# Optimization experiments

Hardware: AMD Instinct MI355X
Metric: run time of the kernel (lower is better)

## Reference

```python
import jax, jax.numpy as jnp
import numpy as np

N = 50000
E = 1600000
NEG_SLOPE = 0.2


def gat_layer(x, src, dst, e_attr, w_fc, w_e, ah, ae, at, b, H, F, act):
    # node projection: [N, H, F]
    feat = (x @ w_fc.T).reshape(N, H, F)
    eh = (feat * ah).sum(-1)          # [N, H] attn_h . feat_src
    et = (feat * at).sum(-1)          # [N, H] attn_t . feat_dst (same feats, homogeneous graph)
    # edge projection: [E, H, F]
    fe = (e_attr @ w_e.T).reshape(E, H, F)
    ee = (fe * ae).sum(-1)            # [E, H]
    # per-edge score: u_add_e then e_add_v, leaky relu
    e = eh[src] + ee + et[dst]        # [E, H]
    e = jnp.where(e > 0, e, NEG_SLOPE * e)
    # edge softmax over incoming edges of each dst node
    m = jax.ops.segment_max(e, dst, num_segments=N)      # [N, H]
    ex = jnp.exp(e - m[dst])
    s = jax.ops.segment_sum(ex, dst, num_segments=N)     # [N, H]
    a = ex / s[dst]                   # [E, H]
    # weighted aggregation: u_mul_e -> sum over incoming edges
    msg = feat[src] * a[:, :, None]   # [E, H, F]
    out = jax.ops.segment_sum(msg, dst, num_segments=N)  # [N, H, F]
    out = out + b.reshape(1, H, F)
    out = out.reshape(N, H * F)       # concat_out=True
    if act:
        out = jax.nn.relu(out)
    return out


def setup_inputs() -> dict:
    key = jax.random.key(0)
    ks = jax.random.split(key, 16)
    d = {}
    d['x'] = jax.random.normal(ks[0], (N, 128), dtype=jnp.float32)
    d['edge_attr'] = jax.random.normal(ks[1], (E, 64), dtype=jnp.float32)
    d['src'] = jax.random.randint(ks[2], (E,), 0, N, dtype=jnp.int32)
    d['dst'] = jax.random.randint(ks[3], (E,), 0, N, dtype=jnp.int32)
    # layer 1: in=128, H=4, F=32
    d['w_fc1'] = jax.random.normal(ks[4], (128, 128), dtype=jnp.float32) * 0.1
    d['w_e1'] = jax.random.normal(ks[5], (128, 64), dtype=jnp.float32) * 0.1
    d['ah1'] = jax.random.normal(ks[6], (4, 32), dtype=jnp.float32) * 0.1
    d['ae1'] = jax.random.normal(ks[7], (4, 32), dtype=jnp.float32) * 0.1
    d['at1'] = jax.random.normal(ks[8], (4, 32), dtype=jnp.float32) * 0.1
    d['b1'] = jnp.zeros((128,), dtype=jnp.float32)
    # layer 2: in=128, H=1, F=64
    d['w_fc2'] = jax.random.normal(ks[9], (64, 128), dtype=jnp.float32) * 0.1
    d['w_e2'] = jax.random.normal(ks[10], (64, 64), dtype=jnp.float32) * 0.1
    d['ah2'] = jax.random.normal(ks[11], (1, 64), dtype=jnp.float32) * 0.1
    d['ae2'] = jax.random.normal(ks[12], (1, 64), dtype=jnp.float32) * 0.1
    d['at2'] = jax.random.normal(ks[13], (1, 64), dtype=jnp.float32) * 0.1
    d['b2'] = jnp.zeros((64,), dtype=jnp.float32)
    return d


def reference(x, edge_attr, src, dst,
              w_fc1, w_e1, ah1, ae1, at1, b1,
              w_fc2, w_e2, ah2, ae2, at2, b2):
    h = gat_layer(x, src, dst, edge_attr, w_fc1, w_e1, ah1, ae1, at1, b1, 4, 32, True)
    h = gat_layer(h, src, dst, edge_attr, w_fc2, w_e2, ah2, ae2, at2, b2, 1, 64, False)
    return h
```

## Files before the change

kernel.cpp:

```cpp
#include <hip/hip_runtime.h>

#define NEG_SLOPE 0.2f

__global__ void hist_k(const int* __restrict__ dst, int* __restrict__ counts,
                       int* __restrict__ pos, int E) {
    int i = blockIdx.x * blockDim.x + threadIdx.x;
    if (i < E) pos[i] = atomicAdd(&counts[dst[i]], 1);
}

__global__ __launch_bounds__(256) void scan_blocks(const int* __restrict__ in,
                                                   int* __restrict__ part,
                                                   int* __restrict__ aux, int n) {
    __shared__ int wsum[4];
    int t = threadIdx.x;
    int lane = t & 63;
    int w = t >> 6;
    int base = blockIdx.x * 1024 + t * 4;
    int c[4];
#pragma unroll
    for (int i = 0; i < 4; ++i) c[i] = (base + i < n) ? in[base + i] : 0;
    int tsum = c[0] + c[1] + c[2] + c[3];
    int incl = tsum;
#pragma unroll
    for (int d = 1; d < 64; d <<= 1) {
        int v = __shfl_up(incl, d, 64);
        if (lane >= d) incl += v;
    }
    if (lane == 63) wsum[w] = incl;
    __syncthreads();
    int wpre = 0;
    for (int i = 0; i < w; ++i) wpre += wsum[i];
    int run = wpre + incl - tsum;
#pragma unroll
    for (int i = 0; i < 4; ++i) {
        if (base + i < n) part[base + i] = run;
        run += c[i];
    }
    if (t == 255) aux[blockIdx.x] = run;
}

__global__ void scan_aux_k(int* __restrict__ aux, int* __restrict__ offs, int nblk, int N) {
    int t = threadIdx.x;
    int v = (t < nblk) ? aux[t] : 0;
    int incl = v;
#pragma unroll
    for (int d = 1; d < 64; d <<= 1) {
        int u = __shfl_up(incl, d, 64);
        if (t >= d) incl += u;
    }
    if (t < nblk) aux[t] = incl - v;
    if (t == 63) offs[N] = incl;
}

__global__ void scan_add_k(int* __restrict__ offs, const int* __restrict__ aux, int n) {
    int i = blockIdx.x * blockDim.x + threadIdx.x;
    if (i < n) offs[i] += aux[i >> 10];
}

__global__ void prep_we(const float* __restrict__ ae1, const float* __restrict__ we1,
                        const float* __restrict__ ae2, const float* __restrict__ we2,
                        float* __restrict__ wec) {
    int t = threadIdx.x;
    if (t < 256) {
        int h = t >> 6, c = t & 63;
        float s = 0.f;
        for (int f = 0; f < 32; ++f) s = fmaf(ae1[h * 32 + f], we1[(h * 32 + f) * 64 + c], s);
        wec[h * 64 + c] = s;
    } else if (t < 320) {
        int c = t - 256;
        float s = 0.f;
        for (int f = 0; f < 64; ++f) s = fmaf(ae2[f], we2[f * 64 + c], s);
        wec[256 + c] = s;
    }
}

__global__ __launch_bounds__(256) void edge_proj_csr(const float* __restrict__ ea,
                                                     const float* __restrict__ wec,
                                                     const float* __restrict__ eh1,
                                                     const int* __restrict__ src,
                                                     const int* __restrict__ dst,
                                                     const int* __restrict__ pos,
                                                     const int* __restrict__ offs,
                                                     float* __restrict__ pe1,
                                                     float* __restrict__ ee2c,
                                                     int* __restrict__ esrc, int E) {
    __shared__ float w[5][64];
    for (int i = threadIdx.x; i < 320; i += 256) w[i / 64][i % 64] = wec[i];
    __syncthreads();
    int e = blockIdx.x * blockDim.x + threadIdx.x;
    if (e >= E) return;
    const float4* row = (const float4*)(ea + (size_t)e * 64);
    float acc[5] = {0.f, 0.f, 0.f, 0.f, 0.f};
#pragma unroll
    for (int q = 0; q < 16; ++q) {
        float4 v = row[q];
#pragma unroll
        for (int h = 0; h < 5; ++h) {
            float4 wv = *(const float4*)&w[h][4 * q];
            acc[h] = fmaf(v.x, wv.x, acc[h]);
            acc[h] = fmaf(v.y, wv.y, acc[h]);
            acc[h] = fmaf(v.z, wv.z, acc[h]);
            acc[h] = fmaf(v.w, wv.w, acc[h]);
        }
    }
    int s = src[e];
    int p = offs[dst[e]] + pos[e];
    float4 ehv = *(const float4*)(eh1 + (size_t)s * 4);
    *(float4*)(pe1 + (size_t)p * 4) =
        make_float4(acc[0] + ehv.x, acc[1] + ehv.y, acc[2] + ehv.z, acc[3] + ehv.w);
    ee2c[p] = acc[4];
    esrc[p] = s;
}

template <int M>
__global__ __launch_bounds__(256) void gemm_nodes(const float* __restrict__ X,
                                                  const float* __restrict__ W,
                                                  float* __restrict__ out, int N) {
    const int K = 128, KC = 64, NT = 64;
    __shared__ float xs[NT][KC + 1];
    __shared__ float ws[KC][M + 1];
    const int CT = M / 8;
    const int NG = 256 / CT;
    const int NPT = NT / NG;
    int t = threadIdx.x;
    int tc = t % CT, tn = t / CT;
    int nb = blockIdx.x * NT;
    float acc[NPT][8];
#pragma unroll
    for (int i = 0; i < NPT; ++i)
#pragma unroll
        for (int j = 0; j < 8; ++j) acc[i][j] = 0.f;

    for (int kc = 0; kc < K; kc += KC) {
        for (int i = t * 4; i < M * KC; i += 1024) {
            int m = i / KC, k = i % KC;
            float4 v = *(const float4*)(W + (size_t)m * K + kc + k);
            ws[k][m] = v.x; ws[k + 1][m] = v.y; ws[k + 2][m] = v.z; ws[k + 3][m] = v.w;
        }
        for (int i = t * 4; i < NT * KC; i += 1024) {
            int r = i / KC, k = i % KC;
            int n = nb + r;
            float4 v = make_float4(0.f, 0.f, 0.f, 0.f);
            if (n < N) v = *(const float4*)(X + (size_t)n * K + kc + k);
            xs[r][k] = v.x; xs[r][k + 1] = v.y; xs[r][k + 2] = v.z; xs[r][k + 3] = v.w;
        }
        __syncthreads();
#pragma unroll 4
        for (int k = 0; k < KC; ++k) {
            float wv[8];
            *(float4*)&wv[0] = *(const float4*)&ws[k][tc * 8];
            *(float4*)&wv[4] = *(const float4*)&ws[k][tc * 8 + 4];
#pragma unroll
            for (int i = 0; i < NPT; ++i) {
                float xv = xs[tn * NPT + i][k];
#pragma unroll
                for (int j = 0; j < 8; ++j) acc[i][j] = fmaf(xv, wv[j], acc[i][j]);
            }
        }
        __syncthreads();
    }
#pragma unroll
    for (int i = 0; i < NPT; ++i) {
        int n = nb + tn * NPT + i;
        if (n < N) {
            *(float4*)(out + (size_t)n * M + tc * 8) =
                make_float4(acc[i][0], acc[i][1], acc[i][2], acc[i][3]);
            *(float4*)(out + (size_t)n * M + tc * 8 + 4) =
                make_float4(acc[i][4], acc[i][5], acc[i][6], acc[i][7]);
        }
    }
}

template <int H, int F>
__global__ void ehet(const float* __restrict__ feat, const float* __restrict__ ah,
                     const float* __restrict__ at, float* __restrict__ eh,
                     float* __restrict__ et, int N) {
    int i = blockIdx.x * blockDim.x + threadIdx.x;
    if (i >= N * H) return;
    int h = i % H;
    const float* f = feat + (size_t)i * F;
    float sh = 0.f, st = 0.f;
#pragma unroll
    for (int j = 0; j < F; j += 4) {
        float4 v = *(const float4*)(f + j);
        float4 a = *(const float4*)(ah + h * F + j);
        float4 b = *(const float4*)(at + h * F + j);
        sh += v.x * a.x + v.y * a.y + v.z * a.z + v.w * a.w;
        st += v.x * b.x + v.y * b.y + v.z * b.z + v.w * b.w;
    }
    eh[i] = sh;
    et[i] = st;
}

__global__ __launch_bounds__(256) void agg1(const float* __restrict__ feat,
                                            const float* __restrict__ pe1,
                                            const float* __restrict__ et,
                                            const int* __restrict__ offs,
                                            const int* __restrict__ esrc,
                                            const float* __restrict__ bias,
                                            float* __restrict__ out, int N) {
    int n = (blockIdx.x * blockDim.x + threadIdx.x) >> 6;
    int l = threadIdx.x & 63;
    if (n >= N) return;
    int start = offs[n], end = offs[n + 1];
    int eg = l >> 3, li = l & 7, h = li >> 1;
    float etv = et[n * 4 + h];

    float s = 0.f;
    float4 a0 = make_float4(0.f, 0.f, 0.f, 0.f);
    float4 a1 = a0, a2 = a0, a3 = a0;
    for (int j0 = start; j0 < end; j0 += 8) {
        int j = j0 + eg;
        if (j < end) {
            int sv = esrc[j];
            float x = pe1[(size_t)j * 4 + h] + etv;
            x = x > 0.f ? x : NEG_SLOPE * x;
            float wgt = __expf(x);
            s += wgt;
            const float4* fr = (const float4*)(feat + (size_t)sv * 128 + li * 16);
            float4 v0 = fr[0], v1 = fr[1], v2 = fr[2], v3 = fr[3];
            a0.x = fmaf(wgt, v0.x, a0.x); a0.y = fmaf(wgt, v0.y, a0.y);
            a0.z = fmaf(wgt, v0.z, a0.z); a0.w = fmaf(wgt, v0.w, a0.w);
            a1.x = fmaf(wgt, v1.x, a1.x); a1.y = fmaf(wgt, v1.y, a1.y);
            a1.z = fmaf(wgt, v1.z, a1.z); a1.w = fmaf(wgt, v1.w, a1.w);
            a2.x = fmaf(wgt, v2.x, a2.x); a2.y = fmaf(wgt, v2.y, a2.y);
            a2.z = fmaf(wgt, v2.z, a2.z); a2.w = fmaf(wgt, v2.w, a2.w);
            a3.x = fmaf(wgt, v3.x, a3.x); a3.y = fmaf(wgt, v3.y, a3.y);
            a3.z = fmaf(wgt, v3.z, a3.z); a3.w = fmaf(wgt, v3.w, a3.w);
        }
    }
#pragma unroll
    for (int d = 8; d < 64; d <<= 1) {
        s += __shfl_xor(s, d);
        a0.x += __shfl_xor(a0.x, d); a0.y += __shfl_xor(a0.y, d);
        a0.z += __shfl_xor(a0.z, d); a0.w += __shfl_xor(a0.w, d);
        a1.x += __shfl_xor(a1.x, d); a1.y += __shfl_xor(a1.y, d);
        a1.z += __shfl_xor(a1.z, d); a1.w += __shfl_xor(a1.w, d);
        a2.x += __shfl_xor(a2.x, d); a2.y += __shfl_xor(a2.y, d);
        a2.z += __shfl_xor(a2.z, d); a2.w += __shfl_xor(a2.w, d);
        a3.x += __shfl_xor(a3.x, d); a3.y += __shfl_xor(a3.y, d);
        a3.z += __shfl_xor(a3.z, d); a3.w += __shfl_xor(a3.w, d);
    }
    if (eg == 0) {
        float inv = s > 0.f ? 1.f / s : 0.f;
        const float4* bp = (const float4*)(bias + li * 16);
        float4 b0 = bp[0], b1 = bp[1], b2 = bp[2], b3 = bp[3];
        float4* op = (float4*)(out + (size_t)n * 128 + li * 16);
        op[0] = make_float4(fmaxf(a0.x * inv + b0.x, 0.f), fmaxf(a0.y * inv + b0.y, 0.f),
                            fmaxf(a0.z * inv + b0.z, 0.f), fmaxf(a0.w * inv + b0.w, 0.f));
        op[1] = make_float4(fmaxf(a1.x * inv + b1.x, 0.f), fmaxf(a1.y * inv + b1.y, 0.f),
                            fmaxf(a1.z * inv + b1.z, 0.f), fmaxf(a1.w * inv + b1.w, 0.f));
        op[2] = make_float4(fmaxf(a2.x * inv + b2.x, 0.f), fmaxf(a2.y * inv + b2.y, 0.f),
                            fmaxf(a2.z * inv + b2.z, 0.f), fmaxf(a2.w * inv + b2.w, 0.f));
        op[3] = make_float4(fmaxf(a3.x * inv + b3.x, 0.f), fmaxf(a3.y * inv + b3.y, 0.f),
                            fmaxf(a3.z * inv + b3.z, 0.f), fmaxf(a3.w * inv + b3.w, 0.f));
    }
}

__global__ __launch_bounds__(256) void agg2(const float* __restrict__ feat,
                                            const float* __restrict__ ee2c,
                                            const float* __restrict__ eh2,
                                            const float* __restrict__ et2,
                                            const int* __restrict__ offs,
                                            const int* __restrict__ esrc,
                                            const float* __restrict__ bias,
                                            float* __restrict__ out, int N) {
    int n = (blockIdx.x * blockDim.x + threadIdx.x) >> 6;
    int l = threadIdx.x & 63;
    if (n >= N) return;
    int start = offs[n], end = offs[n + 1];
    int eg = l >> 3, li = l & 7;
    float etv = et2[n];

    float s = 0.f;
    float4 a0 = make_float4(0.f, 0.f, 0.f, 0.f);
    float4 a1 = a0;
    for (int j0 = start; j0 < end; j0 += 8) {
        int j = j0 + eg;
        if (j < end) {
            int sv = esrc[j];
            float x = eh2[sv] + ee2c[j] + etv;
            x = x > 0.f ? x : NEG_SLOPE * x;
            float wgt = __expf(x);
            s += wgt;
            const float4* fr = (const float4*)(feat + (size_t)sv * 64 + li * 8);
            float4 v0 = fr[0], v1 = fr[1];
            a0.x = fmaf(wgt, v0.x, a0.x); a0.y = fmaf(wgt, v0.y, a0.y);
            a0.z = fmaf(wgt, v0.z, a0.z); a0.w = fmaf(wgt, v0.w, a0.w);
            a1.x = fmaf(wgt, v1.x, a1.x); a1.y = fmaf(wgt, v1.y, a1.y);
            a1.z = fmaf(wgt, v1.z, a1.z); a1.w = fmaf(wgt, v1.w, a1.w);
        }
    }
#pragma unroll
    for (int d = 8; d < 64; d <<= 1) {
        s += __shfl_xor(s, d);
        a0.x += __shfl_xor(a0.x, d); a0.y += __shfl_xor(a0.y, d);
        a0.z += __shfl_xor(a0.z, d); a0.w += __shfl_xor(a0.w, d);
        a1.x += __shfl_xor(a1.x, d); a1.y += __shfl_xor(a1.y, d);
        a1.z += __shfl_xor(a1.z, d); a1.w += __shfl_xor(a1.w, d);
    }
    if (eg == 0) {
        float inv = s > 0.f ? 1.f / s : 0.f;
        const float4* bp = (const float4*)(bias + li * 8);
        float4 b0 = bp[0], b1 = bp[1];
        float4* op = (float4*)(out + (size_t)n * 64 + li * 8);
        op[0] = make_float4(a0.x * inv + b0.x, a0.y * inv + b0.y,
                            a0.z * inv + b0.z, a0.w * inv + b0.w);
        op[1] = make_float4(a1.x * inv + b1.x, a1.y * inv + b1.y,
                            a1.z * inv + b1.z, a1.w * inv + b1.w);
    }
}

extern "C" void kernel_launch(void* const* d_in, const int* in_sizes, int n_in,
                              void* d_out, int out_size, void* d_ws, size_t ws_size,
                              hipStream_t stream) {
    const float* x    = (const float*)d_in[0];
    const float* ea   = (const float*)d_in[1];
    const int*   src  = (const int*)d_in[2];
    const int*   dst  = (const int*)d_in[3];
    const float* wfc1 = (const float*)d_in[4];
    const float* we1  = (const float*)d_in[5];
    const float* ah1  = (const float*)d_in[6];
    const float* ae1  = (const float*)d_in[7];
    const float* at1  = (const float*)d_in[8];
    const float* b1   = (const float*)d_in[9];
    const float* wfc2 = (const float*)d_in[10];
    const float* we2  = (const float*)d_in[11];
    const float* ah2  = (const float*)d_in[12];
    const float* ae2  = (const float*)d_in[13];
    const float* at2  = (const float*)d_in[14];
    const float* b2   = (const float*)d_in[15];
    const int N = in_sizes[0] / 128;
    const int E = in_sizes[2];
    float* out = (float*)d_out;

    char* p = (char*)d_ws;
    auto alloc = [&](size_t bytes) -> void* {
        void* r = (void*)p;
        p += (bytes + 255) & ~(size_t)255;
        return r;
    };
    int*   counts = (int*)alloc((size_t)N * 4);
    int*   offs   = (int*)alloc(((size_t)N + 1) * 4);
    int*   aux    = (int*)alloc(64 * 4);
    int*   pos    = (int*)alloc((size_t)E * 4);
    float* wec    = (float*)alloc(320 * 4);
    float* pe1    = (float*)alloc((size_t)E * 4 * 4);
    float* ee2c   = (float*)alloc((size_t)E * 4);
    int*   esrc   = (int*)alloc((size_t)E * 4);
    float* feat1  = (float*)alloc((size_t)N * 128 * 4);
    float* eh1    = (float*)alloc((size_t)N * 4 * 4);
    float* et1    = (float*)alloc((size_t)N * 4 * 4);
    float* h1     = (float*)alloc((size_t)N * 128 * 4);
    float* feat2  = (float*)alloc((size_t)N * 64 * 4);
    float* eh2    = (float*)alloc((size_t)N * 4);
    float* et2    = (float*)alloc((size_t)N * 4);

    int ebl = (E + 255) / 256;
    int nblk = (N + 1023) / 1024;

    hipMemsetAsync(counts, 0, (size_t)N * 4, stream);
    hist_k<<<ebl, 256, 0, stream>>>(dst, counts, pos, E);
    scan_blocks<<<nblk, 256, 0, stream>>>(counts, offs, aux, N);
    scan_aux_k<<<1, 64, 0, stream>>>(aux, offs, nblk, N);
    scan_add_k<<<(N + 255) / 256, 256, 0, stream>>>(offs, aux, N);

    gemm_nodes<128><<<(N + 63) / 64, 256, 0, stream>>>(x, wfc1, feat1, N);
    ehet<4, 32><<<(N * 4 + 255) / 256, 256, 0, stream>>>(feat1, ah1, at1, eh1, et1, N);

    prep_we<<<1, 320, 0, stream>>>(ae1, we1, ae2, we2, wec);
    edge_proj_csr<<<ebl, 256, 0, stream>>>(ea, wec, eh1, src, dst, pos, offs,
                                           pe1, ee2c, esrc, E);

    agg1<<<(N + 3) / 4, 256, 0, stream>>>(feat1, pe1, et1, offs, esrc, b1, h1, N);

    gemm_nodes<64><<<(N + 63) / 64, 256, 0, stream>>>(h1, wfc2, feat2, N);
    ehet<1, 64><<<(N + 255) / 256, 256, 0, stream>>>(feat2, ah2, at2, eh2, et2, N);
    agg2<<<(N + 3) / 4, 256, 0, stream>>>(feat2, ee2c, eh2, et2, offs, esrc, b2, out, N);
}
```

Baseline: 1.064 ms.

## Coalesce edge projection: 16 lanes per edge row with shuffle reduction

Rewrites the edge projection so each group of 16 lanes reads one 64-float edge row as contiguous float4 loads, with weights held in registers, and reduces the five dot products with xor shuffles. It uses a grid-stride loop over a fixed 4096-block grid, with four edges per lane group per iteration to keep several loads in flight. This targets the uncoalesced per-thread row reads of the 410MB edge_attr stream. The cost is extra shuffle work and lane-0-only scatter stores. A shuffle order swap in agg1 is cosmetic.

Measured after the change: 1.025 ms. -3.7%, faster.

```diff
diff --git a/kernel.cpp b/kernel.cpp
--- a/kernel.cpp
+++ b/kernel.cpp
@@ -84,32 +84,54 @@
                                                      float* __restrict__ pe1,
                                                      float* __restrict__ ee2c,
                                                      int* __restrict__ esrc, int E) {
-    __shared__ float w[5][64];
-    for (int i = threadIdx.x; i < 320; i += 256) w[i / 64][i % 64] = wec[i];
-    __syncthreads();
-    int e = blockIdx.x * blockDim.x + threadIdx.x;
-    if (e >= E) return;
-    const float4* row = (const float4*)(ea + (size_t)e * 64);
-    float acc[5] = {0.f, 0.f, 0.f, 0.f, 0.f};
-#pragma unroll
-    for (int q = 0; q < 16; ++q) {
-        float4 v = row[q];
-#pragma unroll
-        for (int h = 0; h < 5; ++h) {
-            float4 wv = *(const float4*)&w[h][4 * q];
-            acc[h] = fmaf(v.x, wv.x, acc[h]);
-            acc[h] = fmaf(v.y, wv.y, acc[h]);
-            acc[h] = fmaf(v.z, wv.z, acc[h]);
-            acc[h] = fmaf(v.w, wv.w, acc[h]);
-        }
-    }
-    int s = src[e];
-    int p = offs[dst[e]] + pos[e];
-    float4 ehv = *(const float4*)(eh1 + (size_t)s * 4);
-    *(float4*)(pe1 + (size_t)p * 4) =
-        make_float4(acc[0] + ehv.x, acc[1] + ehv.y, acc[2] + ehv.z, acc[3] + ehv.w);
-    ee2c[p] = acc[4];
-    esrc[p] = s;
+    int l = threadIdx.x & 63;
+    int li = l & 15;
+    int eg = l >> 4;
+    int wid = (blockIdx.x * blockDim.x + threadIdx.x) >> 6;
+    int nw = (gridDim.x * blockDim.x) >> 6;
+    float4 w0 = *(const float4*)(wec + 0 * 64 + li * 4);
+    float4 w1 = *(const float4*)(wec + 1 * 64 + li * 4);
+    float4 w2 = *(const float4*)(wec + 2 * 64 + li * 4);
+    float4 w3 = *(const float4*)(wec + 3 * 64 + li * 4);
+    float4 w4 = *(const float4*)(wec + 4 * 64 + li * 4);
+    int nq = (E + 3) >> 2;
+    for (int q0 = wid * 4; q0 < nq; q0 += nw * 4) {
+        float4 v[4];
+        int e[4];
+#pragma unroll
+        for (int u = 0; u < 4; ++u) {
+            e[u] = (q0 + u) * 4 + eg;
+            v[u] = make_float4(0.f, 0.f, 0.f, 0.f);
+            if (e[u] < E) v[u] = *(const float4*)(ea + (size_t)e[u] * 64 + li * 4);
+        }
+#pragma unroll
+        for (int u = 0; u < 4; ++u) {
+            float4 vv = v[u];
+            float d0 = fmaf(vv.x, w0.x, fmaf(vv.y, w0.y, fmaf(vv.z, w0.z, vv.w * w0.w)));
+            float d1 = fmaf(vv.x, w1.x, fmaf(vv.y, w1.y, fmaf(vv.z, w1.z, vv.w * w1.w)));
+            float d2 = fmaf(vv.x, w2.x, fmaf(vv.y, w2.y, fmaf(vv.z, w2.z, vv.w * w2.w)));
+            float d3 = fmaf(vv.x, w3.x, fmaf(vv.y, w3.y, fmaf(vv.z, w3.z, vv.w * w3.w)));
+            float d4 = fmaf(vv.x, w4.x, fmaf(vv.y, w4.y, fmaf(vv.z, w4.z, vv.w * w4.w)));
+#pragma unroll
+            for (int m = 1; m < 16; m <<= 1) {
+                d0 += __shfl_xor(d0, m, 64);
+                d1 += __shfl_xor(d1, m, 64);
+                d2 += __shfl_xor(d2, m, 64);
+                d3 += __shfl_xor(d3, m, 64);
+                d4 += __shfl_xor(d4, m, 64);
+            }
+            if (li == 0 && e[u] < E) {
+                int ee = e[u];
+                int s = src[ee];
+                int p = offs[dst[ee]] + pos[ee];
+                float4 ehv = *(const float4*)(eh1 + (size_t)s * 4);
+                *(float4*)(pe1 + (size_t)p * 4) =
+                    make_float4(d0 + ehv.x, d1 + ehv.y, d2 + ehv.z, d3 + ehv.w);
+                ee2c[p] = d4;
+                esrc[p] = s;
+            }
+        }
+    }
 }
 
 template <int M>
@@ -239,7 +261,7 @@
         a2.x += __shfl_xor(a2.x, d); a2.y += __shfl_xor(a2.y, d);
         a2.z += __shfl_xor(a2.z, d); a2.w += __shfl_xor(a2.w, d);
         a3.x += __shfl_xor(a3.x, d); a3.y += __shfl_xor(a3.y, d);
-        a3.z += __shfl_xor(a3.z, d); a3.w += __shfl_xor(a3.w, d);
+        a3.w += __shfl_xor(a3.w, d); a3.z += __shfl_xor(a3.z, d);
     }
     if (eg == 0) {
         float inv = s > 0.f ? 1.f / s : 0.f;
@@ -369,8 +391,8 @@
     ehet<4, 32><<<(N * 4 + 255) / 256, 256, 0, stream>>>(feat1, ah1, at1, eh1, et1, N);
 
     prep_we<<<1, 320, 0, stream>>>(ae1, we1, ae2, we2, wec);
-    edge_proj_csr<<<ebl, 256, 0, stream>>>(ea, wec, eh1, src, dst, pos, offs,
-                                           pe1, ee2c, esrc, E);
+    edge_proj_csr<<<4096, 256, 0, stream>>>(ea, wec, eh1, src, dst, pos, offs,
+                                            pe1, ee2c, esrc, E);
 
     agg1<<<(N + 3) / 4, 256, 0, stream>>>(feat1, pe1, et1, offs, esrc, b1, h1, N);
 
```
